# Performance work log

Hardware: AMD Instinct MI355X
Metric: run time of the kernel (lower is better)

Reference implementation:

```python
import jax, jax.numpy as jnp
import numpy as np

B, TX, TZ, DX, DZ, DATT, DMID, H, DOUT = 8, 1024, 1024, 1024, 1024, 64, 64, 16, 1024


def setup_inputs() -> dict:
    key = jax.random.key(0)
    ks = jax.random.split(key, 10)
    s = 0.02
    return {
        "x": jax.random.normal(ks[0], (B, TX, DX), jnp.float32),
        "z": jax.random.normal(ks[1], (B, TZ, DZ), jnp.float32),
        "Wq": jax.random.normal(ks[2], (H, DX, DATT), jnp.float32) * s,
        "bq": jax.random.normal(ks[3], (H, DATT), jnp.float32) * s,
        "Wk": jax.random.normal(ks[4], (H, DZ, DATT), jnp.float32) * s,
        "bk": jax.random.normal(ks[5], (H, DATT), jnp.float32) * s,
        "Wv": jax.random.normal(ks[6], (H, DZ, DMID), jnp.float32) * s,
        "bv": jax.random.normal(ks[7], (H, DMID), jnp.float32) * s,
        "Wp": jax.random.normal(ks[8], (H * DMID, DOUT), jnp.float32) * s,
        "bp": jax.random.normal(ks[9], (DOUT,), jnp.float32) * s,
        "mask": jnp.tril(jnp.ones((TX, TZ), dtype=bool)),  # causal
    }


def reference(x, z, Wq, bq, Wk, bk, Wv, bv, Wp, bp, mask):
    # Per-head projections (heads batched via stacked weights). bhxe = batch, head, x-pos, feat
    Q = jnp.einsum('bxd,hde->bhxe', x, Wq) + bq[None, :, None, :]
    K = jnp.einsum('bzd,hde->bhze', z, Wk) + bk[None, :, None, :]
    V = jnp.einsum('bzd,hde->bhze', z, Wv) + bv[None, :, None, :]
    # Scores, mask (set ~mask to -inf), then scale by 1/sqrt(Datt) (as original: mask before scale)
    S = jnp.einsum('bhxe,bhze->bhxz', Q, K)
    S = jnp.where(mask[None, None, :, :], S, -jnp.inf) * (1.0 / jnp.sqrt(jnp.asarray(DATT, S.dtype)))
    A = jax.nn.softmax(S, axis=-1)
    y = jnp.einsum('bhxz,bhze->bhxe', A, V)          # [B, H, Tx, Dmid]
    y_concat = y.transpose(0, 2, 1, 3).reshape(B, TX, H * DMID)  # concat heads
    return y_concat @ Wp + bp
```

## Files before the change

### kernel.cpp

```cpp
#include <hip/hip_runtime.h>
#include <stdint.h>


typedef float    f32x4  __attribute__((ext_vector_type(4)));
typedef __bf16   bf16x8 __attribute__((ext_vector_type(8)));
typedef unsigned short u16x4 __attribute__((ext_vector_type(4)));
typedef unsigned short u16x8 __attribute__((ext_vector_type(8)));

#define MASKNEG (-3.0e38f)
#define QSCALE_F (0.125f * 1.4426950408889634f)

__device__ __forceinline__ unsigned short f2bf(float f) {
  unsigned int u = __float_as_uint(f);
  u += 0x7fffu + ((u >> 16) & 1u);
  return (unsigned short)(u >> 16);
}

__device__ __forceinline__ void gload16(const void* g, void* s) {
  const __attribute__((address_space(1))) unsigned int* gp =
      (const __attribute__((address_space(1))) unsigned int*)(uintptr_t)g;
  __attribute__((address_space(3))) unsigned int* lp =
      (__attribute__((address_space(3))) unsigned int*)(unsigned int)(uintptr_t)s;
  __builtin_amdgcn_global_load_lds(gp, lp, 16, 0, 0);
}

__device__ __forceinline__ f32x4 mfma16(bf16x8 a, bf16x8 b, f32x4 c) {
  return __builtin_amdgcn_mfma_f32_16x16x32_bf16(a, b, c, 0, 0, 0);
}


__global__ __launch_bounds__(256) void k_cvt2(const float* __restrict__ x,
                                              const float* __restrict__ z,
                                              unsigned short* __restrict__ out) {
  int i = blockIdx.x * 256 + threadIdx.x;
  const int stride = gridDim.x * 256;
  for (; i < 2097152; i += stride) {
    const float* in = (i < 1048576) ? (x + (size_t)i * 8) : (z + (size_t)(i - 1048576) * 8);
    const f32x4* p = (const f32x4*)in;
    f32x4 a = p[0], b = p[1];
    u16x8 o;
    o[0] = f2bf(a[0]); o[1] = f2bf(a[1]); o[2] = f2bf(a[2]); o[3] = f2bf(a[3]);
    o[4] = f2bf(b[0]); o[5] = f2bf(b[1]); o[6] = f2bf(b[2]); o[7] = f2bf(b[3]);
    *(u16x8*)(out + (size_t)i * 8) = o;
  }
}

__global__ __launch_bounds__(256) void k_pack(const float* __restrict__ Wq,
                                              const float* __restrict__ Wk,
                                              const float* __restrict__ Wv,
                                              const float* __restrict__ Wp,
                                              unsigned short* __restrict__ Oq,
                                              unsigned short* __restrict__ Ok,
                                              unsigned short* __restrict__ Ov,
                                              unsigned short* __restrict__ Op) {
  __shared__ float tile[64][65];
  const int t = threadIdx.x;
  const int zid = blockIdx.z;
  if (zid < 3) {
    const float* W = zid == 0 ? Wq : (zid == 1 ? Wk : Wv);
    unsigned short* O = zid == 0 ? Oq : (zid == 1 ? Ok : Ov);
    const int h = blockIdx.x, d0 = blockIdx.y * 64;
    const int ee = t & 63, r0 = t >> 6;
#pragma unroll
    for (int dd = r0; dd < 64; dd += 4)
      tile[dd][ee] = W[(h * 1024 + d0 + dd) * 64 + ee];
    __syncthreads();
    const int d = t & 63, e0 = t >> 6;
#pragma unroll
    for (int e = e0; e < 64; e += 4)
      O[(h * 64 + e) * 1024 + d0 + d] = f2bf(tile[d][e]);
  } else {
    const int k0 = blockIdx.x * 64, n0 = blockIdx.y * 64;
    const int nn = t & 63, r0 = t >> 6;
#pragma unroll
    for (int kk = r0; kk < 64; kk += 4)
      tile[kk][nn] = Wp[(k0 + kk) * 1024 + n0 + nn];
    __syncthreads();
    const int kk = t & 63, e0 = t >> 6;
#pragma unroll
    for (int n2 = e0; n2 < 64; n2 += 4)
      Op[(n0 + n2) * 1024 + k0 + kk] = f2bf(tile[kk][n2]);
  }
}

__device__ __forceinline__ void gemm_body(const unsigned short* __restrict__ A,
                                          const unsigned short* __restrict__ Bt,
                                          const float* __restrict__ bias,
                                          void* __restrict__ outp,
                                          int mode, float oscale,
                                          int brow, int bcol,
                                          unsigned short* As, unsigned short* Bs) {
  const int tid = threadIdx.x;
  const int l = tid & 63, w = tid >> 6;
  const int lrow = l & 15, lk = l >> 4;
  const int wr = (w >> 1) * 64, wc = (w & 1) * 64;

  const int arow = tid >> 2;
  const int asrc = ((tid & 3) ^ ((arow >> 1) & 3)) * 8;
  const unsigned short* ag0 = A + (brow + arow) * 1024 + asrc;
  const unsigned short* ag1 = ag0 + 64 * 1024;
  const unsigned short* bg0 = Bt + (bcol + arow) * 1024 + asrc;
  const unsigned short* bg1 = bg0 + 64 * 1024;

  int aoff[4], boff[4];
#pragma unroll
  for (int m = 0; m < 4; m++) {
    int row = wr + m * 16 + lrow;
    aoff[m] = row * 64 + ((lk ^ ((row >> 1) & 3)) << 4);
    int col = wc + m * 16 + lrow;
    boff[m] = col * 64 + ((lk ^ ((col >> 1) & 3)) << 4);
  }

  f32x4 acc[4][4];
#pragma unroll
  for (int n = 0; n < 4; n++) {
    float bv = bias[bcol + wc + n * 16 + lrow];
#pragma unroll
    for (int m = 0; m < 4; m++) acc[m][n] = (f32x4){bv, bv, bv, bv};
  }

  {
    char* asb = (char*)As + w * 1024;
    char* bsb = (char*)Bs + w * 1024;
    gload16(ag0, asb);
    gload16(ag1, asb + 4096);
    gload16(bg0, bsb);
    gload16(bg1, bsb + 4096);
  }
  __syncthreads();

#pragma unroll 2
  for (int kt = 0; kt < 32; kt++) {
    const int cur = kt & 1;
    if (kt < 31) {
      char* asb = (char*)As + (cur ^ 1) * 8192 + w * 1024;
      char* bsb = (char*)Bs + (cur ^ 1) * 8192 + w * 1024;
      gload16(ag0 + (kt + 1) * 32, asb);
      gload16(ag1 + (kt + 1) * 32, asb + 4096);
      gload16(bg0 + (kt + 1) * 32, bsb);
      gload16(bg1 + (kt + 1) * 32, bsb + 4096);
    }
    const char* ab = (const char*)As + cur * 8192;
    const char* bb = (const char*)Bs + cur * 8192;
    bf16x8 af[4], bfr[4];
#pragma unroll
    for (int m = 0; m < 4; m++) af[m] = *(const bf16x8*)(ab + aoff[m]);
#pragma unroll
    for (int n = 0; n < 4; n++) bfr[n] = *(const bf16x8*)(bb + boff[n]);
#pragma unroll
    for (int m = 0; m < 4; m++)
#pragma unroll
      for (int n = 0; n < 4; n++)
        acc[m][n] = mfma16(af[m], bfr[n], acc[m][n]);
    __syncthreads();
  }

  if (mode == 0) {
    unsigned short* C = (unsigned short*)outp;
#pragma unroll
    for (int m = 0; m < 4; m++) {
      int r = brow + wr + m * 16 + 4 * lk;
#pragma unroll
      for (int n = 0; n < 4; n++) {
        int c = bcol + wc + n * 16 + lrow;
        unsigned short* p = C + ((r >> 10) * 16 + (c >> 6)) * 65536 + (r & 1023) * 64 + (c & 63);
#pragma unroll
        for (int j = 0; j < 4; j++) p[j * 64] = f2bf(acc[m][n][j] * oscale);
      }
    }
  } else if (mode == 2) {
    unsigned short* C = (unsigned short*)outp;
#pragma unroll
    for (int m = 0; m < 4; m++) {
      int r = brow + wr + m * 16 + 4 * lk;
#pragma unroll
      for (int n = 0; n < 4; n++) {
        int c = bcol + wc + n * 16 + lrow;
        u16x4 o;
#pragma unroll
        for (int j = 0; j < 4; j++) o[j] = f2bf(acc[m][n][j]);
        *(u16x4*)(C + ((r >> 10) * 16 + (c >> 6)) * 65536 + (c & 63) * 1024 + (r & 1023)) = o;
      }
    }
  } else {
    float* C = (float*)outp;
#pragma unroll
    for (int m = 0; m < 4; m++) {
      int r = brow + wr + m * 16 + 4 * lk;
#pragma unroll
      for (int n = 0; n < 4; n++) {
        int c = bcol + wc + n * 16 + lrow;
#pragma unroll
        for (int j = 0; j < 4; j++) C[(r + j) * 1024 + c] = acc[m][n][j];
      }
    }
  }
}

__global__ __launch_bounds__(256) void k_gemm_qkv(const unsigned short* __restrict__ Xb,
                                                  const unsigned short* __restrict__ Zb,
                                                  const unsigned short* __restrict__ Wqkv,
                                                  const float* __restrict__ bq,
                                                  const float* __restrict__ bk,
                                                  const float* __restrict__ bv,
                                                  unsigned short* __restrict__ Qp,
                                                  unsigned short* __restrict__ Kp,
                                                  unsigned short* __restrict__ Vtp) {
  __shared__ unsigned short As[8192];
  __shared__ unsigned short Bs[8192];
  const int brow = blockIdx.x * 128;
  const int cg = blockIdx.y;
  const int seg = cg >> 3;
  const int bcol = (cg & 7) * 128;
  const unsigned short* A = (seg == 0) ? Xb : Zb;
  const unsigned short* Bt = Wqkv + (size_t)seg * 1048576;
  const float* bias = (seg == 0) ? bq : (seg == 1 ? bk : bv);
  void* outp = (seg == 0) ? (void*)Qp : (seg == 1 ? (void*)Kp : (void*)Vtp);
  const int mode = (seg == 2) ? 2 : 0;
  const float oscale = (seg == 0) ? QSCALE_F : 1.0f;
  gemm_body(A, Bt, bias, outp, mode, oscale, brow, bcol, As, Bs);
}

__global__ __launch_bounds__(256) void k_gemm(const unsigned short* __restrict__ A,
                                              const unsigned short* __restrict__ Bt,
                                              const float* __restrict__ bias,
                                              void* __restrict__ outp,
                                              int mode, float oscale) {
  __shared__ unsigned short As[8192];
  __shared__ unsigned short Bs[8192];
  gemm_body(A, Bt, bias, outp, mode, oscale, blockIdx.x * 128, blockIdx.y * 128, As, Bs);
}

__global__ __launch_bounds__(256) void k_attn(const unsigned short* __restrict__ Qh,
                                              const unsigned short* __restrict__ Kh,
                                              const unsigned short* __restrict__ Vth,
                                              unsigned short* __restrict__ Y) {
  __shared__ unsigned short Ks[8192];
  __shared__ unsigned short Vs[8192];
  __shared__ unsigned short Ps[8192];

  const int tid = threadIdx.x, l = tid & 63, w = tid >> 6;
  const int lrow = l & 15, lk = l >> 4;
  const int bh = blockIdx.y;
  const int pp = blockIdx.x;

  const unsigned short* Qb = Qh + bh * 65536;
  const unsigned short* Kb = Kh + bh * 65536;
  const unsigned short* Vb = Vth + bh * 65536;

  bf16x8 ones;
#pragma unroll
  for (int j = 0; j < 8; j++) ones[j] = (__bf16)1.0f;

  const int srow = tid >> 3;
  const int swz = ((tid & 7) ^ (srow & 7)) * 8;
  const unsigned short* kg0 = Kb + srow * 64 + swz;
  const unsigned short* kg1 = Kb + (srow + 32) * 64 + swz;
  const unsigned short* vg0 = Vb + srow * 1024 + swz;
  const unsigned short* vg1 = Vb + (srow + 32) * 1024 + swz;
  char* pw = (char*)Ps + w * 4096;

  const int b = bh >> 4, h = bh & 15;

#pragma unroll 1
  for (int half = 0; half < 2; half++) {
    const int qi = half == 0 ? (7 - pp) : pp;
    const int qw = qi * 128 + w * 32;
    const int qmax = qw + 31;

    bf16x8 qf[2][2];
#pragma unroll
    for (int qn = 0; qn < 2; qn++) {
      const unsigned short* qp = Qb + (qw + qn * 16 + lrow) * 64 + lk * 8;
      qf[qn][0] = *(const bf16x8*)qp;
      qf[qn][1] = *(const bf16x8*)(qp + 32);
    }

    f32x4 m[2], lsum[2], yacc[2][4];
#pragma unroll
    for (int qn = 0; qn < 2; qn++) {
      m[qn] = (f32x4){MASKNEG, MASKNEG, MASKNEG, MASKNEG};
      lsum[qn] = (f32x4){0.f, 0.f, 0.f, 0.f};
#pragma unroll
      for (int ef = 0; ef < 4; ef++) yacc[qn][ef] = (f32x4){0.f, 0.f, 0.f, 0.f};
    }

    const int nt = qi * 2 + 2;

    {
      char* ksb = (char*)Ks + w * 1024;
      char* vsb = (char*)Vs + w * 1024;
      gload16(kg0, ksb);
      gload16(kg1, ksb + 4096);
      gload16(vg0, vsb);
      gload16(vg1, vsb + 4096);
    }
    __syncthreads();

#pragma unroll 1
    for (int t = 0; t < nt; t++) {
      const int z0 = t * 64;
      const int cur = t & 1;
      if (t < nt - 1) {
        const int zn = (t + 1) * 64;
        char* ksb = (char*)Ks + (cur ^ 1) * 8192 + w * 1024;
        char* vsb = (char*)Vs + (cur ^ 1) * 8192 + w * 1024;
        gload16(kg0 + zn * 64, ksb);
        gload16(kg1 + zn * 64, ksb + 4096);
        gload16(vg0 + zn, vsb);
        gload16(vg1 + zn, vsb + 4096);
      }

      if (z0 <= qmax) {
        const char* kbase = (const char*)Ks + cur * 8192;
        const char* vbase = (const char*)Vs + cur * 8192;

        f32x4 s[2][4];
#pragma unroll
        for (int qn = 0; qn < 2; qn++)
#pragma unroll
          for (int zf = 0; zf < 4; zf++) s[qn][zf] = (f32x4){0.f, 0.f, 0.f, 0.f};
#pragma unroll
        for (int zf = 0; zf < 4; zf++) {
          int zr = zf * 16 + lrow;
#pragma unroll
          for (int kf = 0; kf < 2; kf++) {
            bf16x8 kfr = *(const bf16x8*)(kbase + zr * 128 + (((kf * 4 + lk) ^ (zr & 7)) << 4));
            s[0][zf] = mfma16(qf[0][kf], kfr, s[0][zf]);
            s[1][zf] = mfma16(qf[1][kf], kfr, s[1][zf]);
          }
        }

        if (z0 + 63 > qw) {
#pragma unroll
          for (int qn = 0; qn < 2; qn++) {
            int qbase = qw + qn * 16 + 4 * lk;
#pragma unroll
            for (int zf = 0; zf < 4; zf++) {
              int zg = z0 + zf * 16 + lrow;
#pragma unroll
              for (int j = 0; j < 4; j++)
                if (zg > qbase + j) s[qn][zf][j] = MASKNEG;
            }
          }
        }

#pragma unroll
        for (int qn = 0; qn < 2; qn++) {
#pragma unroll
          for (int j = 0; j < 4; j++) {
            float rm = fmaxf(fmaxf(s[qn][0][j], s[qn][1][j]), fmaxf(s[qn][2][j], s[qn][3][j]));
            rm = fmaxf(rm, __shfl_xor(rm, 1));
            rm = fmaxf(rm, __shfl_xor(rm, 2));
            rm = fmaxf(rm, __shfl_xor(rm, 4));
            rm = fmaxf(rm, __shfl_xor(rm, 8));
            float mn = fmaxf(m[qn][j], rm);
            float a = __builtin_amdgcn_exp2f(m[qn][j] - mn);
            m[qn][j] = mn;
            lsum[qn][j] *= a;
#pragma unroll
            for (int ef = 0; ef < 4; ef++) yacc[qn][ef][j] *= a;
#pragma unroll
            for (int zf = 0; zf < 4; zf++)
              s[qn][zf][j] = __builtin_amdgcn_exp2f(s[qn][zf][j] - mn);
          }

#pragma unroll
          for (int zf = 0; zf < 4; zf++) {
            int zc = zf * 16 + lrow;
            int zp = zc >> 3;
#pragma unroll
            for (int j = 0; j < 4; j++) {
              int q = 4 * lk + j;
              *(unsigned short*)(pw + (qn * 16 + q) * 128 + ((zp ^ (q & 7)) << 4) + (zc & 7) * 2)
                  = f2bf(s[qn][zf][j]);
            }
          }
        }

        asm volatile("s_waitcnt lgkmcnt(0)" ::: "memory");
        __builtin_amdgcn_sched_barrier(0);

        bf16x8 pf[2][2];
#pragma unroll
        for (int qn = 0; qn < 2; qn++)
#pragma unroll
          for (int kf = 0; kf < 2; kf++)
            pf[qn][kf] = *(const bf16x8*)(pw + (qn * 16 + lrow) * 128 + (((kf * 4 + lk) ^ (lrow & 7)) << 4));

#pragma unroll
        for (int qn = 0; qn < 2; qn++)
#pragma unroll
          for (int kf = 0; kf < 2; kf++)
            lsum[qn] = mfma16(pf[qn][kf], ones, lsum[qn]);

#pragma unroll
        for (int ef = 0; ef < 4; ef++) {
          int er = ef * 16 + lrow;
#pragma unroll
          for (int kf = 0; kf < 2; kf++) {
            bf16x8 vf = *(const bf16x8*)(vbase + er * 128 + (((kf * 4 + lk) ^ (er & 7)) << 4));
            yacc[0][ef] = mfma16(pf[0][kf], vf, yacc[0][ef]);
            yacc[1][ef] = mfma16(pf[1][kf], vf, yacc[1][ef]);
          }
        }
      }

      __syncthreads();
    }

#pragma unroll
    for (int qn = 0; qn < 2; qn++) {
      f32x4 rinv;
#pragma unroll
      for (int j = 0; j < 4; j++) rinv[j] = 1.0f / lsum[qn][j];
#pragma unroll
      for (int ef = 0; ef < 4; ef++) {
        int col = h * 64 + ef * 16 + lrow;
#pragma unroll
        for (int j = 0; j < 4; j++) {
          int x = qw + qn * 16 + lk * 4 + j;
          Y[(b * 1024 + x) * 1024 + col] = f2bf(yacc[qn][ef][j] * rinv[j]);
        }
      }
    }
  }
}

extern "C" void kernel_launch(void* const* d_in, const int* in_sizes, int n_in,
                              void* d_out, int out_size, void* d_ws, size_t ws_size,
                              hipStream_t stream) {
  const float* x  = (const float*)d_in[0];
  const float* z  = (const float*)d_in[1];
  const float* Wq = (const float*)d_in[2];
  const float* bq = (const float*)d_in[3];
  const float* Wk = (const float*)d_in[4];
  const float* bk = (const float*)d_in[5];
  const float* Wv = (const float*)d_in[6];
  const float* bv = (const float*)d_in[7];
  const float* Wp = (const float*)d_in[8];
  const float* bp = (const float*)d_in[9];
  (void)in_sizes; (void)n_in; (void)out_size; (void)ws_size;

  char* ws = (char*)d_ws;
  unsigned short* Xb  = (unsigned short*)(ws + 0);
  unsigned short* Zb  = (unsigned short*)(ws + 16777216);
  unsigned short* Wqt = (unsigned short*)(ws + 33554432);
  unsigned short* Wkt = (unsigned short*)(ws + 35651584);
  unsigned short* Wvt = (unsigned short*)(ws + 37748736);
  unsigned short* Wpt = (unsigned short*)(ws + 39845888);
  unsigned short* Qp  = (unsigned short*)(ws + 41943040);
  unsigned short* Kp  = (unsigned short*)(ws + 58720256);
  unsigned short* Vtp = (unsigned short*)(ws + 75497472);

  k_cvt2<<<dim3(2048), dim3(256), 0, stream>>>(x, z, Xb);
  k_pack<<<dim3(16, 16, 4), dim3(256), 0, stream>>>(Wq, Wk, Wv, Wp, Wqt, Wkt, Wvt, Wpt);

  k_gemm_qkv<<<dim3(64, 24), dim3(256), 0, stream>>>(Xb, Zb, Wqt, bq, bk, bv, Qp, Kp, Vtp);

  k_attn<<<dim3(4, 128), dim3(256), 0, stream>>>(Qp, Kp, Vtp, Xb );

  k_gemm<<<dim3(64, 8), dim3(256), 0, stream>>>(Xb, Wpt, bp, d_out, 3, 1.0f);
}
```

Before: 175.2 us.

## Triple-buffer GEMM LDS tiles with two-stage-ahead async prefetch

Moves the shared GEMM body from double buffering to a three-slot LDS ring. Global-to-LDS loads are issued two K-steps ahead, and each step waits with a partial vmcnt plus a raw s_barrier instead of a full __syncthreads. This is meant to hide global load latency behind the MFMA work. In exchange, LDS use per block grows from 32 KB to 48 KB, which may lower occupancy, and correctness now depends on the hand-written waitcnt accounting.

```diff
diff --git a/kernel.cpp b/kernel.cpp
--- a/kernel.cpp
+++ b/kernel.cpp
@@ -119,29 +119,32 @@
     for (int m = 0; m < 4; m++) acc[m][n] = (f32x4){bv, bv, bv, bv};
   }
 
-  {
-    char* asb = (char*)As + w * 1024;
-    char* bsb = (char*)Bs + w * 1024;
-    gload16(ag0, asb);
-    gload16(ag1, asb + 4096);
-    gload16(bg0, bsb);
-    gload16(bg1, bsb + 4096);
-  }
-  __syncthreads();
-
-#pragma unroll 2
+#pragma unroll
+  for (int p = 0; p < 2; p++) {
+    char* asb = (char*)As + p * 8192 + w * 1024;
+    char* bsb = (char*)Bs + p * 8192 + w * 1024;
+    gload16(ag0 + p * 32, asb);
+    gload16(ag1 + p * 32, asb + 4096);
+    gload16(bg0 + p * 32, bsb);
+    gload16(bg1 + p * 32, bsb + 4096);
+  }
+  asm volatile("s_waitcnt vmcnt(4)" ::: "memory");
+  __builtin_amdgcn_s_barrier();
+  __builtin_amdgcn_sched_barrier(0);
+
+  int s0 = 0, s2 = 2;
+#pragma unroll 1
   for (int kt = 0; kt < 32; kt++) {
-    const int cur = kt & 1;
-    if (kt < 31) {
-      char* asb = (char*)As + (cur ^ 1) * 8192 + w * 1024;
-      char* bsb = (char*)Bs + (cur ^ 1) * 8192 + w * 1024;
-      gload16(ag0 + (kt + 1) * 32, asb);
-      gload16(ag1 + (kt + 1) * 32, asb + 4096);
-      gload16(bg0 + (kt + 1) * 32, bsb);
-      gload16(bg1 + (kt + 1) * 32, bsb + 4096);
-    }
-    const char* ab = (const char*)As + cur * 8192;
-    const char* bb = (const char*)Bs + cur * 8192;
+    if (kt < 30) {
+      char* asb = (char*)As + s2 * 8192 + w * 1024;
+      char* bsb = (char*)Bs + s2 * 8192 + w * 1024;
+      gload16(ag0 + (kt + 2) * 32, asb);
+      gload16(ag1 + (kt + 2) * 32, asb + 4096);
+      gload16(bg0 + (kt + 2) * 32, bsb);
+      gload16(bg1 + (kt + 2) * 32, bsb + 4096);
+    }
+    const char* ab = (const char*)As + s0 * 8192;
+    const char* bb = (const char*)Bs + s0 * 8192;
     bf16x8 af[4], bfr[4];
 #pragma unroll
     for (int m = 0; m < 4; m++) af[m] = *(const bf16x8*)(ab + aoff[m]);
@@ -152,7 +155,18 @@
 #pragma unroll
       for (int n = 0; n < 4; n++)
         acc[m][n] = mfma16(af[m], bfr[n], acc[m][n]);
-    __syncthreads();
+
+    if (kt < 31) {
+      if (kt < 30) {
+        asm volatile("s_waitcnt vmcnt(4)" ::: "memory");
+      } else {
+        asm volatile("s_waitcnt vmcnt(0)" ::: "memory");
+      }
+      __builtin_amdgcn_s_barrier();
+      __builtin_amdgcn_sched_barrier(0);
+    }
+    s0 = (s0 == 2) ? 0 : s0 + 1;
+    s2 = (s2 == 2) ? 0 : s2 + 1;
   }
 
   if (mode == 0) {
@@ -206,8 +220,8 @@
                                                   unsigned short* __restrict__ Qp,
                                                   unsigned short* __restrict__ Kp,
                                                   unsigned short* __restrict__ Vtp) {
-  __shared__ unsigned short As[8192];
-  __shared__ unsigned short Bs[8192];
+  __shared__ unsigned short As[12288];
+  __shared__ unsigned short Bs[12288];
   const int brow = blockIdx.x * 128;
   const int cg = blockIdx.y;
   const int seg = cg >> 3;
@@ -226,8 +240,8 @@
                                               const float* __restrict__ bias,
                                               void* __restrict__ outp,
                                               int mode, float oscale) {
-  __shared__ unsigned short As[8192];
-  __shared__ unsigned short Bs[8192];
+  __shared__ unsigned short As[12288];
+  __shared__ unsigned short Bs[12288];
   gemm_body(A, Bt, bias, outp, mode, oscale, blockIdx.x * 128, blockIdx.y * 128, As, Bs);
 }
 
```

Result: no change. 171.9 us (-1.9%).
